# Performance work log

Measured on AMD Instinct MI355X. Metric: run time of the kernel, lower is better.

Reference implementation:

```python
import jax, jax.numpy as jnp
import numpy as np

B, L, D, KSIZE = 16, 2048, 128, 8  # batch, seq_len, d_model (=input=hidden), window size


def setup_inputs() -> dict:
    key = jax.random.key(0)
    ks = jax.random.split(key, 5)
    s = 1.0 / np.sqrt(D)  # PyTorch RNN init range
    return {
        "x": jax.random.normal(ks[0], (B, L, D), jnp.float32),
        "W_ih": jax.random.uniform(ks[1], (3 * D, D), jnp.float32, -s, s),
        "W_hh": jax.random.uniform(ks[2], (3 * D, D), jnp.float32, -s, s),
        "b_ih": jax.random.uniform(ks[3], (3 * D,), jnp.float32, -s, s),
        "b_hh": jax.random.uniform(ks[4], (3 * D,), jnp.float32, -s, s),
    }


def _local_gru(x, W_ih, W_hh, b_ih, b_hh, ksize):
    # x: [B, L, D]. Equivalent to get_K (left zero-pad + sliding windows of
    # length ksize) followed by a GRU over each window, keeping the last
    # hidden state. Instead of materializing [B*L, ksize, D] windows, we scan
    # over the ksize window positions: at step t, every window reads the
    # shifted sequence x_pad[:, t:t+L, :].
    Bb, Ll, Dd = x.shape
    H = W_hh.shape[1]
    pad = jnp.zeros((Bb, ksize - 1, Dd), x.dtype)
    xp = jnp.concatenate([pad, x], axis=1)  # [B, L+k-1, D]
    xs = jnp.stack([xp[:, t:t + Ll, :] for t in range(ksize)], axis=0)  # [k, B, L, D]

    Wir, Wiz, Win = jnp.split(W_ih, 3, axis=0)
    Whr, Whz, Whn = jnp.split(W_hh, 3, axis=0)
    bir, biz, bin_ = jnp.split(b_ih, 3)
    bhr, bhz, bhn = jnp.split(b_hh, 3)

    def step(h, xt):  # h, xt: [B, L, H/D]
        r = jax.nn.sigmoid(xt @ Wir.T + bir + h @ Whr.T + bhr)
        z = jax.nn.sigmoid(xt @ Wiz.T + biz + h @ Whz.T + bhz)
        n = jnp.tanh(xt @ Win.T + bin_ + r * (h @ Whn.T + bhn))
        h = (1.0 - z) * n + z * h
        return h, None

    h0 = jnp.zeros((Bb, Ll, H), x.dtype)
    h_last, _ = jax.lax.scan(step, h0, xs)
    return h_last  # [B, L, H]: last hidden state of each length-ksize window


def reference(x, W_ih, W_hh, b_ih, b_hh):
    return _local_gru(x, W_ih, W_hh, b_ih, b_hh, KSIZE)
```

## Files before the change

kernel.cpp:

```cpp
#include <hip/hip_runtime.h>

#define DEV __device__ __forceinline__

typedef __attribute__((ext_vector_type(8))) short bf16x8;
typedef __attribute__((ext_vector_type(4))) float f32x4;

constexpr int Bq = 16, Lq = 2048, Dq = 128, KW = 8;
constexpr int G3 = 3 * Dq;

DEV unsigned short f2bf(float f) {
    unsigned u = __float_as_uint(f);
    return (unsigned short)((u + 0x7FFFu + ((u >> 16) & 1u)) >> 16);
}
DEV float bf2f(unsigned short s) { return __uint_as_float(((unsigned)s) << 16); }

DEV float sigm(float x) { return __builtin_amdgcn_rcpf(1.f + __expf(-x)); }
DEV float tanh_(float x) {
    float e = __expf(2.f * x);
    return 1.f - 2.f * __builtin_amdgcn_rcpf(e + 1.f);
}

DEV bf16x8 pack8(float4 a, float4 b) {
    bf16x8 r;
    r[0] = (short)f2bf(a.x); r[1] = (short)f2bf(a.y);
    r[2] = (short)f2bf(a.z); r[3] = (short)f2bf(a.w);
    r[4] = (short)f2bf(b.x); r[5] = (short)f2bf(b.y);
    r[6] = (short)f2bf(b.z); r[7] = (short)f2bf(b.w);
    return r;
}
DEV int2 packbf4(float a, float b, float c, float d) {
    int2 r;
    r.x = (int)(((unsigned)f2bf(b) << 16) | (unsigned)f2bf(a));
    r.y = (int)(((unsigned)f2bf(d) << 16) | (unsigned)f2bf(c));
    return r;
}

__global__ __launch_bounds__(512, 4) void k_proj(
    const float* __restrict__ x, const float* __restrict__ W_ih,
    const float* __restrict__ b_ih, const float* __restrict__ b_hh,
    unsigned short* __restrict__ Xp)
{
    __shared__ __attribute__((aligned(16))) unsigned char lds[64 * 768];

    const int tid = threadIdx.x;
    const int lane = tid & 63, w = tid >> 6;
    const int l15 = lane & 15, l4 = lane >> 4;
    const int r0 = blockIdx.x * 64;

#pragma unroll
    for (int it = 0; it < 4; ++it) {
        int c = it * 512 + tid;
        int byte = c << 4;
        int row = byte >> 9;
        int wb = byte & 511;
        float4 v = *(const float4*)((const char*)(x + (size_t)r0 * Dq) + byte);
        int dst = row * 256 + ((wb >> 1) ^ ((row & 7) << 4));
        *(int2*)(lds + dst) = packbf4(v.x, v.y, v.z, v.w);
    }

    bf16x8 afr[3][4];
#pragma unroll
    for (int mt = 0; mt < 3; ++mt)
#pragma unroll
        for (int kc = 0; kc < 4; ++kc) {
            int row = 48 * w + 16 * mt + l15;
            int k0 = 32 * kc + 8 * l4;
            const float* p = W_ih + row * Dq + k0;
            afr[mt][kc] = pack8(*(const float4*)p, *(const float4*)(p + 4));
        }
    float bias[3][4];
#pragma unroll
    for (int mt = 0; mt < 3; ++mt)
#pragma unroll
        for (int r = 0; r < 4; ++r) {
            int row = 48 * w + 16 * mt + 4 * l4 + r;
            bias[mt][r] = b_ih[row] + (row < 2 * Dq ? b_hh[row] : 0.f);
        }
    __syncthreads();

    f32x4 acc[3][4];
#pragma unroll
    for (int mt = 0; mt < 3; ++mt)
#pragma unroll
        for (int nt = 0; nt < 4; ++nt) {
            acc[mt][nt][0] = 0.f; acc[mt][nt][1] = 0.f;
            acc[mt][nt][2] = 0.f; acc[mt][nt][3] = 0.f;
        }

#pragma unroll
    for (int kc = 0; kc < 4; ++kc) {
        bf16x8 bfr[4];
#pragma unroll
        for (int nt = 0; nt < 4; ++nt) {
            int row = 16 * nt + l15;
            int off = row * 256 + ((64 * kc + 16 * l4) ^ ((row & 7) << 4));
            bfr[nt] = *(const bf16x8*)(lds + off);
        }
#pragma unroll
        for (int nt = 0; nt < 4; ++nt)
#pragma unroll
            for (int mt = 0; mt < 3; ++mt)
                acc[mt][nt] = __builtin_amdgcn_mfma_f32_16x16x32_bf16(
                    afr[mt][kc], bfr[nt], acc[mt][nt], 0, 0, 0);
    }

    __syncthreads();

#pragma unroll
    for (int mt = 0; mt < 3; ++mt)
#pragma unroll
        for (int nt = 0; nt < 4; ++nt) {
            int r = 16 * nt + l15;
            int g = 48 * w + 16 * mt + 4 * l4;
            int sw = ((r + 7) & 7) << 3;
            int2 pk = packbf4(acc[mt][nt][0] + bias[mt][0],
                              acc[mt][nt][1] + bias[mt][1],
                              acc[mt][nt][2] + bias[mt][2],
                              acc[mt][nt][3] + bias[mt][3]);
            *(int2*)(lds + 2 * (size_t)(r * G3 + (g ^ sw))) = pk;
        }
    __syncthreads();

    {
        int4* dst = (int4*)(Xp + (size_t)r0 * G3);
#pragma unroll
        for (int it = 0; it < 6; ++it)
            dst[it * 512 + tid] = ((const int4*)lds)[it * 512 + tid];
    }
}

__global__ __launch_bounds__(512, 4) void k_rnn(
    const unsigned short* __restrict__ Xp, const float* __restrict__ W_hh,
    const float* __restrict__ b_ih, const float* __restrict__ b_hh,
    float* __restrict__ out)
{
    __shared__ __attribute__((aligned(16))) unsigned char xpt[40 * 768];
    __shared__ __attribute__((aligned(16))) unsigned char hls[32 * 256];

    const int tid = threadIdx.x;
    const int lane = tid & 63, w = tid >> 6;
    const int l15 = lane & 15, l4 = lane >> 4;
    const int b = blockIdx.x >> 6;
    const int l0 = (blockIdx.x & 63) << 5;

    bf16x8 afr[3][4];
#pragma unroll
    for (int g = 0; g < 3; ++g)
#pragma unroll
        for (int kc = 0; kc < 4; ++kc) {
            int row = 128 * g + 16 * w + l15;
            int k0 = 32 * kc + 8 * l4;
            const float* p = W_hh + row * Dq + k0;
            afr[g][kc] = pack8(*(const float4*)p, *(const float4*)(p + 4));
        }
    const int u0 = 16 * w + 4 * l4;
    f32x4 bhn4;
#pragma unroll
    for (int r = 0; r < 4; ++r) bhn4[r] = b_hh[2 * Dq + u0 + r];

    if (l0 == 0) {
        for (int i = tid; i < 7 * G3; i += 512) {
            int tr = i / G3, g = i - tr * G3;
            float v = b_ih[g] + (g < 2 * Dq ? b_hh[g] : 0.f);
            ((unsigned short*)xpt)[tr * G3 + (g ^ ((tr & 7) << 3))] = f2bf(v);
        }
        const int4* src = (const int4*)(Xp + (size_t)b * Lq * G3);
#pragma unroll
        for (int it = 0; it < 3; ++it)
            ((int4*)(xpt + 7 * 768))[it * 512 + tid] = src[it * 512 + tid];
    } else {
        const int4* src = (const int4*)(Xp + ((size_t)b * Lq + l0 - 7) * G3);
        for (int c = tid; c < 39 * 48; c += 512)
            ((int4*)xpt)[c] = src[c];
    }
    __syncthreads();

    f32x4 h[2];

#pragma unroll
    for (int nt = 0; nt < 2; ++nt) {
        int tr = 16 * nt + l15;
        int base = tr * G3;
        int s = (tr & 7) << 3;
        const ushort4 qr = *(const ushort4*)(xpt + 2 * (size_t)(base + ((0 * Dq + u0) ^ s)));
        const ushort4 qz = *(const ushort4*)(xpt + 2 * (size_t)(base + ((1 * Dq + u0) ^ s)));
        const ushort4 qn = *(const ushort4*)(xpt + 2 * (size_t)(base + ((2 * Dq + u0) ^ s)));
        float xr[4] = {bf2f(qr.x), bf2f(qr.y), bf2f(qr.z), bf2f(qr.w)};
        float xz[4] = {bf2f(qz.x), bf2f(qz.y), bf2f(qz.z), bf2f(qz.w)};
        float xn[4] = {bf2f(qn.x), bf2f(qn.y), bf2f(qn.z), bf2f(qn.w)};
#pragma unroll
        for (int r = 0; r < 4; ++r) {
            float rv = sigm(xr[r]);
            float zv = sigm(xz[r]);
            float nv = tanh_(fmaf(rv, bhn4[r], xn[r]));
            h[nt][r] = nv - zv * nv;
        }
    }
#pragma unroll
    for (int nt = 0; nt < 2; ++nt) {
        int win = 16 * nt + l15;
        int off = win * 256 + ((2 * u0) ^ ((win & 7) << 4));
        *(int2*)(hls + off) = packbf4(h[nt][0], h[nt][1], h[nt][2], h[nt][3]);
    }
    __syncthreads();

    for (int t = 1; t < 8; ++t) {
        f32x4 ar[2], az[2], an[2];
#pragma unroll
        for (int nt = 0; nt < 2; ++nt) {
            ar[nt][0] = 0.f; ar[nt][1] = 0.f; ar[nt][2] = 0.f; ar[nt][3] = 0.f;
            az[nt] = ar[nt];
            an[nt] = bhn4;
        }
#pragma unroll
        for (int kc = 0; kc < 4; ++kc) {
            bf16x8 bfr[2];
#pragma unroll
            for (int nt = 0; nt < 2; ++nt) {
                int row = 16 * nt + l15;
                int off = row * 256 + ((64 * kc + 16 * l4) ^ ((row & 7) << 4));
                bfr[nt] = *(const bf16x8*)(hls + off);
            }
#pragma unroll
            for (int nt = 0; nt < 2; ++nt) {
                ar[nt] = __builtin_amdgcn_mfma_f32_16x16x32_bf16(afr[0][kc], bfr[nt], ar[nt], 0, 0, 0);
                az[nt] = __builtin_amdgcn_mfma_f32_16x16x32_bf16(afr[1][kc], bfr[nt], az[nt], 0, 0, 0);
                an[nt] = __builtin_amdgcn_mfma_f32_16x16x32_bf16(afr[2][kc], bfr[nt], an[nt], 0, 0, 0);
            }
        }
#pragma unroll
        for (int nt = 0; nt < 2; ++nt) {
            int tr = 16 * nt + l15 + t;
            int base = tr * G3;
            int s = (tr & 7) << 3;
            const ushort4 qr = *(const ushort4*)(xpt + 2 * (size_t)(base + ((0 * Dq + u0) ^ s)));
            const ushort4 qz = *(const ushort4*)(xpt + 2 * (size_t)(base + ((1 * Dq + u0) ^ s)));
            const ushort4 qn = *(const ushort4*)(xpt + 2 * (size_t)(base + ((2 * Dq + u0) ^ s)));
            float xr[4] = {bf2f(qr.x), bf2f(qr.y), bf2f(qr.z), bf2f(qr.w)};
            float xz[4] = {bf2f(qz.x), bf2f(qz.y), bf2f(qz.z), bf2f(qz.w)};
            float xn[4] = {bf2f(qn.x), bf2f(qn.y), bf2f(qn.z), bf2f(qn.w)};
#pragma unroll
            for (int r = 0; r < 4; ++r) {
                float rv = sigm(ar[nt][r] + xr[r]);
                float zv = sigm(az[nt][r] + xz[r]);
                float nv = tanh_(fmaf(rv, an[nt][r], xn[r]));
                h[nt][r] = nv + zv * (h[nt][r] - nv);
            }
        }
        if (t < 7) {
            __syncthreads();
#pragma unroll
            for (int nt = 0; nt < 2; ++nt) {
                int win = 16 * nt + l15;
                int off = win * 256 + ((2 * u0) ^ ((win & 7) << 4));
                *(int2*)(hls + off) = packbf4(h[nt][0], h[nt][1], h[nt][2], h[nt][3]);
            }
            __syncthreads();
        }
    }

#pragma unroll
    for (int nt = 0; nt < 2; ++nt) {
        size_t idx = ((size_t)(b * Lq + l0 + 16 * nt + l15)) * Dq + u0;
        *(f32x4*)(out + idx) = h[nt];
    }
}

extern "C" void kernel_launch(void* const* d_in, const int* in_sizes, int n_in,
                              void* d_out, int out_size, void* d_ws, size_t ws_size,
                              hipStream_t stream) {
    const float* x    = (const float*)d_in[0];
    const float* W_ih = (const float*)d_in[1];
    const float* W_hh = (const float*)d_in[2];
    const float* b_ih = (const float*)d_in[3];
    const float* b_hh = (const float*)d_in[4];
    float* out = (float*)d_out;
    unsigned short* Xp = (unsigned short*)d_ws;

    k_proj<<<dim3(512), dim3(512), 0, stream>>>(x, W_ih, b_ih, b_hh, Xp);
    k_rnn<<<dim3(1024), dim3(512), 0, stream>>>(Xp, W_hh, b_ih, b_hh, out);
}
```

Baseline: 165.1 us.

## Fold log2e scaling into weights and double windows per RNN block

Pre-scales the W_ih/W_hh weights and biases by log2(e), or 2·log2(e) for the n gate, so the sigmoid and tanh can call the hardware exp2 directly without a multiply. The recurrent kernel now processes 64 windows per block instead of 32, which halves the grid and cuts the 7-row halo overhead and the per-block cost of loading W_hh. It also switches the bf16 rounding to the library conversion. In exchange it raises LDS and register use per block, which can lower occupancy, and leaves fewer blocks to fill the GPU.

```diff
diff --git a/kernel.cpp b/kernel.cpp
--- a/kernel.cpp
+++ b/kernel.cpp
@@ -1,4 +1,5 @@
 #include <hip/hip_runtime.h>
+#include <hip/hip_bf16.h>
 
 #define DEV __device__ __forceinline__
 
@@ -7,25 +8,29 @@
 
 constexpr int Bq = 16, Lq = 2048, Dq = 128, KW = 8;
 constexpr int G3 = 3 * Dq;
+constexpr float L2E = 1.4426950408889634f;
+
+DEV float exp2f_hw(float x) { return __builtin_amdgcn_exp2f(x); }
 
 DEV unsigned short f2bf(float f) {
-    unsigned u = __float_as_uint(f);
-    return (unsigned short)((u + 0x7FFFu + ((u >> 16) & 1u)) >> 16);
+    union { __hip_bfloat16 h; unsigned short u; } v;
+    v.h = __float2bfloat16(f);
+    return v.u;
 }
 DEV float bf2f(unsigned short s) { return __uint_as_float(((unsigned)s) << 16); }
 
-DEV float sigm(float x) { return __builtin_amdgcn_rcpf(1.f + __expf(-x)); }
-DEV float tanh_(float x) {
-    float e = __expf(2.f * x);
-    return 1.f - 2.f * __builtin_amdgcn_rcpf(e + 1.f);
-}
-
-DEV bf16x8 pack8(float4 a, float4 b) {
+DEV float sigm2(float y) { return __builtin_amdgcn_rcpf(1.f + exp2f_hw(-y)); }
+DEV float tanh2(float y) {
+    float e = exp2f_hw(y);
+    return fmaf(-2.f, __builtin_amdgcn_rcpf(e + 1.f), 1.f);
+}
+
+DEV bf16x8 pack8s(float4 a, float4 b, float s) {
     bf16x8 r;
-    r[0] = (short)f2bf(a.x); r[1] = (short)f2bf(a.y);
-    r[2] = (short)f2bf(a.z); r[3] = (short)f2bf(a.w);
-    r[4] = (short)f2bf(b.x); r[5] = (short)f2bf(b.y);
-    r[6] = (short)f2bf(b.z); r[7] = (short)f2bf(b.w);
+    r[0] = (short)f2bf(a.x * s); r[1] = (short)f2bf(a.y * s);
+    r[2] = (short)f2bf(a.z * s); r[3] = (short)f2bf(a.w * s);
+    r[4] = (short)f2bf(b.x * s); r[5] = (short)f2bf(b.y * s);
+    r[6] = (short)f2bf(b.z * s); r[7] = (short)f2bf(b.w * s);
     return r;
 }
 DEV int2 packbf4(float a, float b, float c, float d) {
@@ -66,16 +71,20 @@
             int row = 48 * w + 16 * mt + l15;
             int k0 = 32 * kc + 8 * l4;
             const float* p = W_ih + row * Dq + k0;
-            afr[mt][kc] = pack8(*(const float4*)p, *(const float4*)(p + 4));
-        }
-    float bias[3][4];
-#pragma unroll
-    for (int mt = 0; mt < 3; ++mt)
+            afr[mt][kc] = pack8s(*(const float4*)p, *(const float4*)(p + 4), 1.f);
+        }
+    float fs[3], bias[3][4];
+#pragma unroll
+    for (int mt = 0; mt < 3; ++mt) {
+        int rbase = 48 * w + 16 * mt + 4 * l4;
+        fs[mt] = (rbase < 2 * Dq) ? L2E : 2.f * L2E;
 #pragma unroll
         for (int r = 0; r < 4; ++r) {
-            int row = 48 * w + 16 * mt + 4 * l4 + r;
-            bias[mt][r] = b_ih[row] + (row < 2 * Dq ? b_hh[row] : 0.f);
-        }
+            int row = rbase + r;
+            float bv = b_ih[row] + (row < 2 * Dq ? b_hh[row] : 0.f);
+            bias[mt][r] = bv * fs[mt];
+        }
+    }
     __syncthreads();
 
     f32x4 acc[3][4];
@@ -113,10 +122,10 @@
             int r = 16 * nt + l15;
             int g = 48 * w + 16 * mt + 4 * l4;
             int sw = ((r + 7) & 7) << 3;
-            int2 pk = packbf4(acc[mt][nt][0] + bias[mt][0],
-                              acc[mt][nt][1] + bias[mt][1],
-                              acc[mt][nt][2] + bias[mt][2],
-                              acc[mt][nt][3] + bias[mt][3]);
+            int2 pk = packbf4(fmaf(acc[mt][nt][0], fs[mt], bias[mt][0]),
+                              fmaf(acc[mt][nt][1], fs[mt], bias[mt][1]),
+                              fmaf(acc[mt][nt][2], fs[mt], bias[mt][2]),
+                              fmaf(acc[mt][nt][3], fs[mt], bias[mt][3]));
             *(int2*)(lds + 2 * (size_t)(r * G3 + (g ^ sw))) = pk;
         }
     __syncthreads();
@@ -134,51 +143,54 @@
     const float* __restrict__ b_ih, const float* __restrict__ b_hh,
     float* __restrict__ out)
 {
-    __shared__ __attribute__((aligned(16))) unsigned char xpt[40 * 768];
-    __shared__ __attribute__((aligned(16))) unsigned char hls[32 * 256];
+    __shared__ __attribute__((aligned(16))) unsigned char xpt[71 * 768];
+    __shared__ __attribute__((aligned(16))) unsigned char hls[64 * 256];
 
     const int tid = threadIdx.x;
     const int lane = tid & 63, w = tid >> 6;
     const int l15 = lane & 15, l4 = lane >> 4;
-    const int b = blockIdx.x >> 6;
-    const int l0 = (blockIdx.x & 63) << 5;
+    const int b = blockIdx.x >> 5;
+    const int l0 = (blockIdx.x & 31) << 6;
 
     bf16x8 afr[3][4];
 #pragma unroll
-    for (int g = 0; g < 3; ++g)
+    for (int g = 0; g < 3; ++g) {
+        float fg = (g < 2) ? L2E : 2.f * L2E;
 #pragma unroll
         for (int kc = 0; kc < 4; ++kc) {
             int row = 128 * g + 16 * w + l15;
             int k0 = 32 * kc + 8 * l4;
             const float* p = W_hh + row * Dq + k0;
-            afr[g][kc] = pack8(*(const float4*)p, *(const float4*)(p + 4));
-        }
+            afr[g][kc] = pack8s(*(const float4*)p, *(const float4*)(p + 4), fg);
+        }
+    }
     const int u0 = 16 * w + 4 * l4;
     f32x4 bhn4;
 #pragma unroll
-    for (int r = 0; r < 4; ++r) bhn4[r] = b_hh[2 * Dq + u0 + r];
+    for (int r = 0; r < 4; ++r) bhn4[r] = b_hh[2 * Dq + u0 + r] * (2.f * L2E);
 
     if (l0 == 0) {
         for (int i = tid; i < 7 * G3; i += 512) {
             int tr = i / G3, g = i - tr * G3;
-            float v = b_ih[g] + (g < 2 * Dq ? b_hh[g] : 0.f);
+            float fg = (g < 2 * Dq) ? L2E : 2.f * L2E;
+            float v = (b_ih[g] + (g < 2 * Dq ? b_hh[g] : 0.f)) * fg;
             ((unsigned short*)xpt)[tr * G3 + (g ^ ((tr & 7) << 3))] = f2bf(v);
         }
         const int4* src = (const int4*)(Xp + (size_t)b * Lq * G3);
 #pragma unroll
-        for (int it = 0; it < 3; ++it)
+        for (int it = 0; it < 6; ++it)
             ((int4*)(xpt + 7 * 768))[it * 512 + tid] = src[it * 512 + tid];
     } else {
         const int4* src = (const int4*)(Xp + ((size_t)b * Lq + l0 - 7) * G3);
-        for (int c = tid; c < 39 * 48; c += 512)
+        for (int c = tid; c < 71 * 48; c += 512)
             ((int4*)xpt)[c] = src[c];
     }
     __syncthreads();
 
-    f32x4 h[2];
-
-#pragma unroll
-    for (int nt = 0; nt < 2; ++nt) {
+    f32x4 h[4];
+
+#pragma unroll
+    for (int nt = 0; nt < 4; ++nt) {
         int tr = 16 * nt + l15;
         int base = tr * G3;
         int s = (tr & 7) << 3;
@@ -190,14 +202,14 @@
         float xn[4] = {bf2f(qn.x), bf2f(qn.y), bf2f(qn.z), bf2f(qn.w)};
 #pragma unroll
         for (int r = 0; r < 4; ++r) {
-            float rv = sigm(xr[r]);
-            float zv = sigm(xz[r]);
-            float nv = tanh_(fmaf(rv, bhn4[r], xn[r]));
+            float rv = sigm2(xr[r]);
+            float zv = sigm2(xz[r]);
+            float nv = tanh2(fmaf(rv, bhn4[r], xn[r]));
             h[nt][r] = nv - zv * nv;
         }
     }
 #pragma unroll
-    for (int nt = 0; nt < 2; ++nt) {
+    for (int nt = 0; nt < 4; ++nt) {
         int win = 16 * nt + l15;
         int off = win * 256 + ((2 * u0) ^ ((win & 7) << 4));
         *(int2*)(hls + off) = packbf4(h[nt][0], h[nt][1], h[nt][2], h[nt][3]);
@@ -205,31 +217,31 @@
     __syncthreads();
 
     for (int t = 1; t < 8; ++t) {
-        f32x4 ar[2], az[2], an[2];
-#pragma unroll
-        for (int nt = 0; nt < 2; ++nt) {
+        f32x4 ar[4], az[4], an[4];
+#pragma unroll
+        for (int nt = 0; nt < 4; ++nt) {
             ar[nt][0] = 0.f; ar[nt][1] = 0.f; ar[nt][2] = 0.f; ar[nt][3] = 0.f;
             az[nt] = ar[nt];
             an[nt] = bhn4;
         }
 #pragma unroll
         for (int kc = 0; kc < 4; ++kc) {
-            bf16x8 bfr[2];
-#pragma unroll
-            for (int nt = 0; nt < 2; ++nt) {
+            bf16x8 bfr[4];
+#pragma unroll
+            for (int nt = 0; nt < 4; ++nt) {
                 int row = 16 * nt + l15;
                 int off = row * 256 + ((64 * kc + 16 * l4) ^ ((row & 7) << 4));
                 bfr[nt] = *(const bf16x8*)(hls + off);
             }
 #pragma unroll
-            for (int nt = 0; nt < 2; ++nt) {
+            for (int nt = 0; nt < 4; ++nt) {
                 ar[nt] = __builtin_amdgcn_mfma_f32_16x16x32_bf16(afr[0][kc], bfr[nt], ar[nt], 0, 0, 0);
                 az[nt] = __builtin_amdgcn_mfma_f32_16x16x32_bf16(afr[1][kc], bfr[nt], az[nt], 0, 0, 0);
                 an[nt] = __builtin_amdgcn_mfma_f32_16x16x32_bf16(afr[2][kc], bfr[nt], an[nt], 0, 0, 0);
             }
         }
 #pragma unroll
-        for (int nt = 0; nt < 2; ++nt) {
+        for (int nt = 0; nt < 4; ++nt) {
             int tr = 16 * nt + l15 + t;
             int base = tr * G3;
             int s = (tr & 7) << 3;
@@ -241,16 +253,16 @@
             float xn[4] = {bf2f(qn.x), bf2f(qn.y), bf2f(qn.z), bf2f(qn.w)};
 #pragma unroll
             for (int r = 0; r < 4; ++r) {
-                float rv = sigm(ar[nt][r] + xr[r]);
-                float zv = sigm(az[nt][r] + xz[r]);
-                float nv = tanh_(fmaf(rv, an[nt][r], xn[r]));
+                float rv = sigm2(ar[nt][r] + xr[r]);
+                float zv = sigm2(az[nt][r] + xz[r]);
+                float nv = tanh2(fmaf(rv, an[nt][r], xn[r]));
                 h[nt][r] = nv + zv * (h[nt][r] - nv);
             }
         }
         if (t < 7) {
             __syncthreads();
 #pragma unroll
-            for (int nt = 0; nt < 2; ++nt) {
+            for (int nt = 0; nt < 4; ++nt) {
                 int win = 16 * nt + l15;
                 int off = win * 256 + ((2 * u0) ^ ((win & 7) << 4));
                 *(int2*)(hls + off) = packbf4(h[nt][0], h[nt][1], h[nt][2], h[nt][3]);
@@ -260,7 +272,7 @@
     }
 
 #pragma unroll
-    for (int nt = 0; nt < 2; ++nt) {
+    for (int nt = 0; nt < 4; ++nt) {
         size_t idx = ((size_t)(b * Lq + l0 + 16 * nt + l15)) * Dq + u0;
         *(f32x4*)(out + idx) = h[nt];
     }
@@ -278,5 +290,5 @@
     unsigned short* Xp = (unsigned short*)d_ws;
 
     k_proj<<<dim3(512), dim3(512), 0, stream>>>(x, W_ih, b_ih, b_hh, Xp);
-    k_rnn<<<dim3(1024), dim3(512), 0, stream>>>(Xp, W_hh, b_ih, b_hh, out);
-}
+    k_rnn<<<dim3(512), dim3(512), 0, stream>>>(Xp, W_hh, b_ih, b_hh, out);
+}
```

New measurement: 149.1 us. 1.11x faster.
